# Optimization experiments

Measured on AMD Instinct MI355X. Metric: run time of the kernel, lower is better.

The kernel has to match this reference:

```python
import jax, jax.numpy as jnp
import numpy as np

TOP_K = 2

def setup_inputs() -> dict:
    key = jax.random.key(0)
    ks = jax.random.split(key, 6)
    B, S, D, F, E = 2, 2048, 1024, 4096, 8
    sd = 1.0 / np.sqrt(D)
    sf = 1.0 / np.sqrt(F)
    return {
        "x": jax.random.normal(ks[0], (B, S, D), jnp.float32),
        "gate_w": jax.random.normal(ks[1], (D, E), jnp.float32) * sd,
        "w1": jax.random.normal(ks[2], (E, D, F), jnp.float32) * sd,
        "b1": jax.random.normal(ks[3], (E, F), jnp.float32) * 0.01,
        "w2": jax.random.normal(ks[4], (E, F, D), jnp.float32) * sf,
        "b2": jax.random.normal(ks[5], (E, D), jnp.float32) * 0.01,
    }

def reference(x, gate_w, w1, b1, w2, b2):
    B, S, D = x.shape
    T = B * S
    xf = x.reshape(T, D)
    # gating: softmax over experts, top-k, renormalize
    gate_scores = jax.nn.softmax(xf @ gate_w, axis=-1)          # [T, E]
    topk_scores, topk_idx = jax.lax.top_k(gate_scores, TOP_K)    # [T, K]
    topk_scores = topk_scores / jnp.sum(topk_scores, axis=-1, keepdims=True)
    # all experts applied to all tokens (dense grouped FFN), exact erf GELU as nn.GELU
    h = jax.nn.gelu(jnp.einsum('td,edf->etf', xf, w1) + b1[:, None, :], approximate=False)  # [E,T,F]
    y = jnp.einsum('etf,efd->etd', h, w2) + b2[:, None, :]       # [E,T,D]
    # combine: gather the top-k expert outputs per token, weight and sum
    tok = jnp.arange(T)
    y_sel = y[topk_idx.T, tok[None, :]]                           # [K,T,D]
    out = jnp.einsum('kt,ktd->td', topk_scores.T, y_sel)
    return out.reshape(B, S, D)
```

## Files before the change

kernel.cpp:

```cpp
#include <hip/hip_runtime.h>
#include <hip/hip_bf16.h>
#include <stdint.h>

#define T_TOK 4096
#define D_DIM 1024
#define F_DIM 4096
#define E_NUM 8
#define NROUTED (T_TOK * 2)

typedef __attribute__((ext_vector_type(8))) __bf16 bf16x8;
typedef __attribute__((ext_vector_type(4))) float f32x4;
typedef __attribute__((ext_vector_type(8))) unsigned short u16x8;

#define WS_COUNTS 0
#define WS_CURSORS 64
#define WS_OFFSETS 128
#define WS_TOPKI 4096
#define WS_TOPKW (WS_TOPKI + NROUTED * 4)
#define WS_ROWS (WS_TOPKW + NROUTED * 4)
#define WS_DEST (WS_ROWS + NROUTED * 4)
#define WS_XB ((size_t)1 << 20)
#define WS_W1T (WS_XB + (size_t)T_TOK * D_DIM * 2)
#define WS_W2T (WS_W1T + (size_t)E_NUM * D_DIM * F_DIM * 2)
#define WS_H (WS_W2T + (size_t)E_NUM * D_DIM * F_DIM * 2)
#define WS_Y (WS_H + (size_t)NROUTED * F_DIM * 2)

__device__ __forceinline__ unsigned short f2bf(float f) {
  uint32_t u = __float_as_uint(f);
  uint32_t r = (u + 0x7FFFu + ((u >> 16) & 1u)) >> 16;
  return (unsigned short)r;
}

__device__ __forceinline__ void gll16(const void* g, void* l) {
  __builtin_amdgcn_global_load_lds(
      (__attribute__((address_space(1))) void*)(void*)(g),
      (__attribute__((address_space(3))) void*)(l), 16, 0, 0);
}

__global__ void cast_x_kernel(const float* __restrict__ x, unsigned short* __restrict__ xb) {
  int n4 = T_TOK * D_DIM / 4;
  for (int i = blockIdx.x * blockDim.x + threadIdx.x; i < n4; i += gridDim.x * blockDim.x) {
    float4 v = reinterpret_cast<const float4*>(x)[i];
    ushort4 o;
    o.x = f2bf(v.x); o.y = f2bf(v.y); o.z = f2bf(v.z); o.w = f2bf(v.w);
    reinterpret_cast<ushort4*>(xb)[i] = o;
  }
}

__global__ void transpose_cast_kernel(const float* __restrict__ src,
                                      unsigned short* __restrict__ dst, int R, int C) {
  __shared__ float tile[64][65];
  const int e = blockIdx.z;
  const int c0 = blockIdx.x * 64, r0 = blockIdx.y * 64;
  const float* s = src + (size_t)e * R * C;
  unsigned short* d = dst + (size_t)e * C * R;
  const int t = threadIdx.x;
  const int lr = t >> 4, lc = (t & 15) * 4;
#pragma unroll
  for (int rr = 0; rr < 4; rr++) {
    const int r = lr + rr * 16;
    float4 v = *reinterpret_cast<const float4*>(s + (size_t)(r0 + r) * C + c0 + lc);
    tile[r][lc + 0] = v.x; tile[r][lc + 1] = v.y;
    tile[r][lc + 2] = v.z; tile[r][lc + 3] = v.w;
  }
  __syncthreads();
  const int wc = t >> 3, wr = (t & 7) * 8;
#pragma unroll
  for (int cc = 0; cc < 2; cc++) {
    const int c = wc + cc * 32;
    u16x8 o;
#pragma unroll
    for (int k = 0; k < 8; k++) o[k] = f2bf(tile[wr + k][c]);
    *reinterpret_cast<u16x8*>(d + (size_t)(c0 + c) * R + r0 + wr) = o;
  }
}

__global__ void gate_kernel(const float* __restrict__ x, const float* __restrict__ gw,
                            int* __restrict__ topk_i, float* __restrict__ topk_w,
                            int* __restrict__ counts) {
  const int wave = threadIdx.x >> 6, lane = threadIdx.x & 63;
  const int t = blockIdx.x * 4 + wave;
  const float* xr = x + (size_t)t * D_DIM;
  double acc[E_NUM] = {0, 0, 0, 0, 0, 0, 0, 0};
  for (int d = lane; d < D_DIM; d += 64) {
    double xv = (double)xr[d];
    const float* g = gw + d * E_NUM;
#pragma unroll
    for (int e = 0; e < E_NUM; e++) acc[e] += xv * (double)g[e];
  }
#pragma unroll
  for (int off = 32; off > 0; off >>= 1) {
#pragma unroll
    for (int e = 0; e < E_NUM; e++) acc[e] += __shfl_xor(acc[e], off, 64);
  }
  if (lane == 0) {
    int i0 = 0; double b0 = acc[0];
    for (int e = 1; e < E_NUM; e++) if (acc[e] > b0) { b0 = acc[e]; i0 = e; }
    int i1 = -1; double b1v = -1e300;
    for (int e = 0; e < E_NUM; e++) if (e != i0 && acc[e] > b1v) { b1v = acc[e]; i1 = e; }
    double w0 = 1.0 / (1.0 + exp(b1v - b0));
    topk_i[t * 2] = i0; topk_i[t * 2 + 1] = i1;
    topk_w[t * 2] = (float)w0; topk_w[t * 2 + 1] = (float)(1.0 - w0);
    atomicAdd(&counts[i0], 1); atomicAdd(&counts[i1], 1);
  }
}

__global__ void scan_kernel(const int* __restrict__ counts, int* __restrict__ offsets) {
  if (threadIdx.x == 0) {
    int s = 0;
    for (int e = 0; e < E_NUM; e++) { offsets[e] = s; s += counts[e]; }
  }
}

__global__ void build_lists_kernel(const int* __restrict__ topk_i, const int* __restrict__ offsets,
                                   int* __restrict__ cursors, int* __restrict__ rows,
                                   int* __restrict__ dest) {
  int t = blockIdx.x * blockDim.x + threadIdx.x;
  if (t >= T_TOK) return;
#pragma unroll
  for (int k = 0; k < 2; k++) {
    int e = topk_i[t * 2 + k];
    int slot = atomicAdd(&cursors[e], 1);
    int r = offsets[e] + slot;
    rows[r] = t;
    dest[t * 2 + k] = r;
  }
}

__global__ __launch_bounds__(256, 3) void gemm1_kernel(
    const unsigned short* __restrict__ xb, const unsigned short* __restrict__ w1T,
    const float* __restrict__ b1, const int* __restrict__ counts,
    const int* __restrict__ offsets, const int* __restrict__ rows,
    unsigned short* __restrict__ h) {
  const int hw = blockIdx.x;
  const int lid = (hw & 7) * (8192 >> 3) + (hw >> 3);
  const int nt = lid & 31;
  const int mt = (lid >> 5) & 31;
  const int e = lid >> 10;

  const int cnt = counts[e];
  if (mt * 128 >= cnt) return;
  const int off = offsets[e];
  const int t = threadIdx.x;
  const int lane = t & 63, wave = t >> 6;
  const int wm = wave >> 1, wn = wave & 1;

  __shared__ __align__(16) unsigned short ldsA[3][4096];
  __shared__ __align__(16) unsigned short ldsB[3][4096];

  const int tr = t >> 2, tc = t & 3;
  const int a0 = mt * 128 + tr;
  const int g0 = rows[off + min(a0, cnt - 1)];
  const int g1 = rows[off + min(a0 + 64, cnt - 1)];
  const unsigned short* aptr0 = xb + (size_t)g0 * D_DIM + tc * 8;
  const unsigned short* aptr1 = xb + (size_t)g1 * D_DIM + tc * 8;
  const unsigned short* wb = w1T + (size_t)e * F_DIM * D_DIM;
  const unsigned short* bptr0 = wb + (size_t)(nt * 128 + tr) * D_DIM + tc * 8;
  const unsigned short* bptr1 = bptr0 + (size_t)64 * D_DIM;

  const int col = lane & 15;
  float bias_v[4];
#pragma unroll
  for (int nf = 0; nf < 4; nf++)
    bias_v[nf] = b1[(size_t)e * F_DIM + nt * 128 + wn * 64 + nf * 16 + col];

  f32x4 acc[4][4];
  const f32x4 z = {0.f, 0.f, 0.f, 0.f};
#pragma unroll
  for (int i = 0; i < 4; i++)
#pragma unroll
    for (int j = 0; j < 4; j++) acc[i][j] = z;

  auto stage = [&](int buf, int kt) {
    const int kb = kt * 32;
    gll16(aptr0 + kb, &ldsA[buf][wave * 512]);
    gll16(aptr1 + kb, &ldsA[buf][2048 + wave * 512]);
    gll16(bptr0 + kb, &ldsB[buf][wave * 512]);
    gll16(bptr1 + kb, &ldsB[buf][2048 + wave * 512]);
  };

  asm volatile("s_waitcnt vmcnt(0)" ::: "memory");
  stage(0, 0);
  stage(1, 1);

  const int rA = wm * 64 + (lane & 15);
  const int rB = wn * 64 + (lane & 15);
  const int ko = (lane >> 4) * 8;
  const int NK = D_DIM / 32;

  for (int kt = 0; kt < NK; ++kt) {
    const int cur = kt - (kt / 3) * 3;
    if (kt + 2 < NK) {
      stage((kt + 2) - ((kt + 2) / 3) * 3, kt + 2);
      asm volatile("s_waitcnt vmcnt(8)" ::: "memory");
    } else if (kt + 2 == NK) {
      asm volatile("s_waitcnt vmcnt(4)" ::: "memory");
    } else {
      asm volatile("s_waitcnt vmcnt(0)" ::: "memory");
    }
    __builtin_amdgcn_s_barrier();
    bf16x8 af[4], bfr[4];
#pragma unroll
    for (int mf = 0; mf < 4; mf++)
      af[mf] = *(const bf16x8*)&ldsA[cur][(rA + mf * 16) * 32 + ko];
#pragma unroll
    for (int nf = 0; nf < 4; nf++)
      bfr[nf] = *(const bf16x8*)&ldsB[cur][(rB + nf * 16) * 32 + ko];
#pragma unroll
    for (int mf = 0; mf < 4; mf++)
#pragma unroll
      for (int nf = 0; nf < 4; nf++)
        acc[mf][nf] = __builtin_amdgcn_mfma_f32_16x16x32_bf16(af[mf], bfr[nf], acc[mf][nf], 0, 0, 0);
    __builtin_amdgcn_s_barrier();
  }

  const int valid = cnt - mt * 128;
  const int rq = (lane >> 4) * 4;
#pragma unroll
  for (int nf = 0; nf < 4; nf++) {
    const int c = nt * 128 + wn * 64 + nf * 16 + col;
    const float bias = bias_v[nf];
#pragma unroll
    for (int mf = 0; mf < 4; mf++) {
#pragma unroll
      for (int r4 = 0; r4 < 4; r4++) {
        int rloc = wm * 64 + mf * 16 + rq + r4;
        if (rloc < valid) {
          float v = acc[mf][nf][r4] + bias;
          v = 0.5f * v * (1.0f + erff(v * 0.7071067811865475f));
          h[(size_t)(off + mt * 128 + rloc) * F_DIM + c] = f2bf(v);
        }
      }
    }
  }
}

__global__ __launch_bounds__(256, 3) void gemm2_kernel(
    const unsigned short* __restrict__ h, const unsigned short* __restrict__ w2T,
    const float* __restrict__ b2, const int* __restrict__ counts,
    const int* __restrict__ offsets, float* __restrict__ y) {
  const int hw = blockIdx.x;
  const int lid = (hw & 7) * (2048 >> 3) + (hw >> 3);
  const int nt = lid & 7;
  const int mt = (lid >> 3) & 31;
  const int e = lid >> 8;

  const int cnt = counts[e];
  if (mt * 128 >= cnt) return;
  const int off = offsets[e];
  const int t = threadIdx.x;
  const int lane = t & 63, wave = t >> 6;
  const int wm = wave >> 1, wn = wave & 1;

  __shared__ __align__(16) unsigned short ldsA[3][4096];
  __shared__ __align__(16) unsigned short ldsB[3][4096];

  const int tr = t >> 2, tc = t & 3;
  const int l0 = min(mt * 128 + tr, cnt - 1);
  const int l1 = min(mt * 128 + 64 + tr, cnt - 1);
  const unsigned short* aptr0 = h + (size_t)(off + l0) * F_DIM + tc * 8;
  const unsigned short* aptr1 = h + (size_t)(off + l1) * F_DIM + tc * 8;
  const unsigned short* wb = w2T + (size_t)e * D_DIM * F_DIM;
  const unsigned short* bptr0 = wb + (size_t)(nt * 128 + tr) * F_DIM + tc * 8;
  const unsigned short* bptr1 = bptr0 + (size_t)64 * F_DIM;

  const int col = lane & 15;
  float bias_v[4];
#pragma unroll
  for (int nf = 0; nf < 4; nf++)
    bias_v[nf] = b2[(size_t)e * D_DIM + nt * 128 + wn * 64 + nf * 16 + col];

  f32x4 acc[4][4];
  const f32x4 z = {0.f, 0.f, 0.f, 0.f};
#pragma unroll
  for (int i = 0; i < 4; i++)
#pragma unroll
    for (int j = 0; j < 4; j++) acc[i][j] = z;

  auto stage = [&](int buf, int kt) {
    const int kb = kt * 32;
    gll16(aptr0 + kb, &ldsA[buf][wave * 512]);
    gll16(aptr1 + kb, &ldsA[buf][2048 + wave * 512]);
    gll16(bptr0 + kb, &ldsB[buf][wave * 512]);
    gll16(bptr1 + kb, &ldsB[buf][2048 + wave * 512]);
  };

  asm volatile("s_waitcnt vmcnt(0)" ::: "memory");
  stage(0, 0);
  stage(1, 1);

  const int rA = wm * 64 + (lane & 15);
  const int rB = wn * 64 + (lane & 15);
  const int ko = (lane >> 4) * 8;
  const int NK = F_DIM / 32;

  for (int kt = 0; kt < NK; ++kt) {
    const int cur = kt - (kt / 3) * 3;
    if (kt + 2 < NK) {
      stage((kt + 2) - ((kt + 2) / 3) * 3, kt + 2);
      asm volatile("s_waitcnt vmcnt(8)" ::: "memory");
    } else if (kt + 2 == NK) {
      asm volatile("s_waitcnt vmcnt(4)" ::: "memory");
    } else {
      asm volatile("s_waitcnt vmcnt(0)" ::: "memory");
    }
    __builtin_amdgcn_s_barrier();
    bf16x8 af[4], bfr[4];
#pragma unroll
    for (int mf = 0; mf < 4; mf++)
      af[mf] = *(const bf16x8*)&ldsA[cur][(rA + mf * 16) * 32 + ko];
#pragma unroll
    for (int nf = 0; nf < 4; nf++)
      bfr[nf] = *(const bf16x8*)&ldsB[cur][(rB + nf * 16) * 32 + ko];
#pragma unroll
    for (int mf = 0; mf < 4; mf++)
#pragma unroll
      for (int nf = 0; nf < 4; nf++)
        acc[mf][nf] = __builtin_amdgcn_mfma_f32_16x16x32_bf16(af[mf], bfr[nf], acc[mf][nf], 0, 0, 0);
    __builtin_amdgcn_s_barrier();
  }

  const int valid = cnt - mt * 128;
  const int rq = (lane >> 4) * 4;
#pragma unroll
  for (int nf = 0; nf < 4; nf++) {
    const int c = nt * 128 + wn * 64 + nf * 16 + col;
    const float bias = bias_v[nf];
#pragma unroll
    for (int mf = 0; mf < 4; mf++) {
#pragma unroll
      for (int r4 = 0; r4 < 4; r4++) {
        int rloc = wm * 64 + mf * 16 + rq + r4;
        if (rloc < valid)
          y[(size_t)(off + mt * 128 + rloc) * D_DIM + c] = acc[mf][nf][r4] + bias;
      }
    }
  }
}

__global__ void combine_kernel(const float* __restrict__ y, const int* __restrict__ dest,
                               const float* __restrict__ tw, float* __restrict__ out) {
  const int n4 = T_TOK * D_DIM / 4;
  for (int i = blockIdx.x * blockDim.x + threadIdx.x; i < n4; i += gridDim.x * blockDim.x) {
    int tok = i >> 8;
    int c = i & 255;
    int r0 = dest[2 * tok], r1 = dest[2 * tok + 1];
    float w0 = tw[2 * tok], w1 = tw[2 * tok + 1];
    float4 a = reinterpret_cast<const float4*>(y + (size_t)r0 * D_DIM)[c];
    float4 b = reinterpret_cast<const float4*>(y + (size_t)r1 * D_DIM)[c];
    float4 o;
    o.x = w0 * a.x + w1 * b.x; o.y = w0 * a.y + w1 * b.y;
    o.z = w0 * a.z + w1 * b.z; o.w = w0 * a.w + w1 * b.w;
    reinterpret_cast<float4*>(out + (size_t)tok * D_DIM)[c] = o;
  }
}

extern "C" void kernel_launch(void* const* d_in, const int* in_sizes, int n_in,
                              void* d_out, int out_size, void* d_ws, size_t ws_size,
                              hipStream_t stream) {
  (void)in_sizes; (void)n_in; (void)out_size; (void)ws_size;
  const float* x = (const float*)d_in[0];
  const float* gw = (const float*)d_in[1];
  const float* w1 = (const float*)d_in[2];
  const float* b1 = (const float*)d_in[3];
  const float* w2 = (const float*)d_in[4];
  const float* b2 = (const float*)d_in[5];
  float* out = (float*)d_out;
  char* ws = (char*)d_ws;

  int* counts = (int*)(ws + WS_COUNTS);
  int* cursors = (int*)(ws + WS_CURSORS);
  int* offsets = (int*)(ws + WS_OFFSETS);
  int* topk_i = (int*)(ws + WS_TOPKI);
  float* topk_w = (float*)(ws + WS_TOPKW);
  int* rows = (int*)(ws + WS_ROWS);
  int* dest = (int*)(ws + WS_DEST);
  unsigned short* xb = (unsigned short*)(ws + WS_XB);
  unsigned short* w1T = (unsigned short*)(ws + WS_W1T);
  unsigned short* w2T = (unsigned short*)(ws + WS_W2T);
  unsigned short* hbuf = (unsigned short*)(ws + WS_H);
  float* ybuf = (float*)(ws + WS_Y);

  hipMemsetAsync(ws, 0, 4096, stream);
  cast_x_kernel<<<2048, 256, 0, stream>>>(x, xb);
  gate_kernel<<<T_TOK / 4, 256, 0, stream>>>(x, gw, topk_i, topk_w, counts);
  scan_kernel<<<1, 64, 0, stream>>>(counts, offsets);
  build_lists_kernel<<<T_TOK / 256, 256, 0, stream>>>(topk_i, offsets, cursors, rows, dest);
  transpose_cast_kernel<<<dim3(F_DIM / 64, D_DIM / 64, E_NUM), 256, 0, stream>>>(w1, w1T, D_DIM, F_DIM);
  gemm1_kernel<<<8192, 256, 0, stream>>>(xb, w1T, b1, counts, offsets, rows, hbuf);
  transpose_cast_kernel<<<dim3(D_DIM / 64, F_DIM / 64, E_NUM), 256, 0, stream>>>(w2, w2T, F_DIM, D_DIM);
  gemm2_kernel<<<2048, 256, 0, stream>>>(hbuf, w2T, b2, counts, offsets, ybuf);
  combine_kernel<<<2048, 256, 0, stream>>>(ybuf, dest, topk_w, out);
}
```

Before: 702.6 us.

## Fuse x cast into gating, deterministic compaction, swizzle LDS, stage gemm1 output via LDS

Folds the bf16 cast of x into the gate kernel and replaces the scan and atomic list build with one ballot-based compaction kernel per expert, removing two launches and an extra pass over x. Both GEMMs get an XOR swizzle on the LDS k-chunk layout to cut bank conflicts on fragment reads, and the ring-buffer index uses counters instead of modulo. The gemm1 epilogue writes GELU results into LDS and stores full 16-byte rows, which coalesces the h writes at the cost of an extra barrier. The compaction kernel walks all tokens serially per expert on one wave, which could add latency.

Result: faster. 667.4 us (-5.0%).

```diff
diff --git a/kernel.cpp b/kernel.cpp
--- a/kernel.cpp
+++ b/kernel.cpp
@@ -13,7 +13,6 @@
 typedef __attribute__((ext_vector_type(8))) unsigned short u16x8;
 
 #define WS_COUNTS 0
-#define WS_CURSORS 64
 #define WS_OFFSETS 128
 #define WS_TOPKI 4096
 #define WS_TOPKW (WS_TOPKI + NROUTED * 4)
@@ -37,16 +36,6 @@
       (__attribute__((address_space(3))) void*)(l), 16, 0, 0);
 }
 
-__global__ void cast_x_kernel(const float* __restrict__ x, unsigned short* __restrict__ xb) {
-  int n4 = T_TOK * D_DIM / 4;
-  for (int i = blockIdx.x * blockDim.x + threadIdx.x; i < n4; i += gridDim.x * blockDim.x) {
-    float4 v = reinterpret_cast<const float4*>(x)[i];
-    ushort4 o;
-    o.x = f2bf(v.x); o.y = f2bf(v.y); o.z = f2bf(v.z); o.w = f2bf(v.w);
-    reinterpret_cast<ushort4*>(xb)[i] = o;
-  }
-}
-
 __global__ void transpose_cast_kernel(const float* __restrict__ src,
                                       unsigned short* __restrict__ dst, int R, int C) {
   __shared__ float tile[64][65];
@@ -76,17 +65,27 @@
 }
 
 __global__ void gate_kernel(const float* __restrict__ x, const float* __restrict__ gw,
+                            unsigned short* __restrict__ xb,
                             int* __restrict__ topk_i, float* __restrict__ topk_w,
                             int* __restrict__ counts) {
   const int wave = threadIdx.x >> 6, lane = threadIdx.x & 63;
   const int t = blockIdx.x * 4 + wave;
   const float* xr = x + (size_t)t * D_DIM;
+  unsigned short* xo = xb + (size_t)t * D_DIM;
   double acc[E_NUM] = {0, 0, 0, 0, 0, 0, 0, 0};
-  for (int d = lane; d < D_DIM; d += 64) {
-    double xv = (double)xr[d];
-    const float* g = gw + d * E_NUM;
-#pragma unroll
-    for (int e = 0; e < E_NUM; e++) acc[e] += xv * (double)g[e];
+#pragma unroll
+  for (int it = 0; it < D_DIM / 256; it++) {
+    const int d0 = it * 256 + lane * 4;
+    float4 v = *reinterpret_cast<const float4*>(xr + d0);
+    ushort4 o;
+    o.x = f2bf(v.x); o.y = f2bf(v.y); o.z = f2bf(v.z); o.w = f2bf(v.w);
+    *reinterpret_cast<ushort4*>(xo + d0) = o;
+    const float* g = gw + (size_t)d0 * E_NUM;
+    float xv[4] = {v.x, v.y, v.z, v.w};
+#pragma unroll
+    for (int j = 0; j < 4; j++)
+#pragma unroll
+      for (int e = 0; e < E_NUM; e++) acc[e] += (double)xv[j] * (double)g[j * E_NUM + e];
   }
 #pragma unroll
   for (int off = 32; off > 0; off >>= 1) {
@@ -105,27 +104,30 @@
   }
 }
 
-__global__ void scan_kernel(const int* __restrict__ counts, int* __restrict__ offsets) {
-  if (threadIdx.x == 0) {
-    int s = 0;
-    for (int e = 0; e < E_NUM; e++) { offsets[e] = s; s += counts[e]; }
-  }
-}
-
-__global__ void build_lists_kernel(const int* __restrict__ topk_i, const int* __restrict__ offsets,
-                                   int* __restrict__ cursors, int* __restrict__ rows,
-                                   int* __restrict__ dest) {
-  int t = blockIdx.x * blockDim.x + threadIdx.x;
-  if (t >= T_TOK) return;
-#pragma unroll
-  for (int k = 0; k < 2; k++) {
-    int e = topk_i[t * 2 + k];
-    int slot = atomicAdd(&cursors[e], 1);
-    int r = offsets[e] + slot;
-    rows[r] = t;
-    dest[t * 2 + k] = r;
-  }
-}
+__global__ void compact_kernel(const int* __restrict__ topk_i, const int* __restrict__ counts,
+                               int* __restrict__ offsets, int* __restrict__ rows,
+                               int* __restrict__ dest) {
+  const int e = blockIdx.x;
+  const int lane = threadIdx.x;
+  int offv = 0;
+  for (int i = 0; i < e; i++) offv += counts[i];
+  if (lane == 0) offsets[e] = offv;
+  int run = 0;
+  for (int c = 0; c < T_TOK; c += 64) {
+    const int t = c + lane;
+    const int i0 = topk_i[2 * t], i1 = topk_i[2 * t + 1];
+    const bool hit = (i0 == e) || (i1 == e);
+    unsigned long long m = __ballot(hit);
+    int pre = __popcll(m & ((1ull << lane) - 1ull));
+    if (hit) {
+      int r = offv + run + pre;
+      rows[r] = t;
+      dest[2 * t + (i0 == e ? 0 : 1)] = r;
+    }
+    run += __popcll(m);
+  }
+}
+
 
 __global__ __launch_bounds__(256, 3) void gemm1_kernel(
     const unsigned short* __restrict__ xb, const unsigned short* __restrict__ w1T,
@@ -145,17 +147,19 @@
   const int lane = t & 63, wave = t >> 6;
   const int wm = wave >> 1, wn = wave & 1;
 
-  __shared__ __align__(16) unsigned short ldsA[3][4096];
-  __shared__ __align__(16) unsigned short ldsB[3][4096];
-
-  const int tr = t >> 2, tc = t & 3;
+  __shared__ __align__(16) unsigned short lds[24576];
+  unsigned short* ldsA = lds;
+  unsigned short* ldsB = lds + 12288;
+
+  const int tr = t >> 2;
+  const int tcs = (t & 3) ^ ((t >> 3) & 3);
   const int a0 = mt * 128 + tr;
   const int g0 = rows[off + min(a0, cnt - 1)];
   const int g1 = rows[off + min(a0 + 64, cnt - 1)];
-  const unsigned short* aptr0 = xb + (size_t)g0 * D_DIM + tc * 8;
-  const unsigned short* aptr1 = xb + (size_t)g1 * D_DIM + tc * 8;
+  const unsigned short* aptr0 = xb + (size_t)g0 * D_DIM + tcs * 8;
+  const unsigned short* aptr1 = xb + (size_t)g1 * D_DIM + tcs * 8;
   const unsigned short* wb = w1T + (size_t)e * F_DIM * D_DIM;
-  const unsigned short* bptr0 = wb + (size_t)(nt * 128 + tr) * D_DIM + tc * 8;
+  const unsigned short* bptr0 = wb + (size_t)(nt * 128 + tr) * D_DIM + tcs * 8;
   const unsigned short* bptr1 = bptr0 + (size_t)64 * D_DIM;
 
   const int col = lane & 15;
@@ -173,10 +177,10 @@
 
   auto stage = [&](int buf, int kt) {
     const int kb = kt * 32;
-    gll16(aptr0 + kb, &ldsA[buf][wave * 512]);
-    gll16(aptr1 + kb, &ldsA[buf][2048 + wave * 512]);
-    gll16(bptr0 + kb, &ldsB[buf][wave * 512]);
-    gll16(bptr1 + kb, &ldsB[buf][2048 + wave * 512]);
+    gll16(aptr0 + kb, ldsA + buf * 4096 + wave * 512);
+    gll16(aptr1 + kb, ldsA + buf * 4096 + 2048 + wave * 512);
+    gll16(bptr0 + kb, ldsB + buf * 4096 + wave * 512);
+    gll16(bptr1 + kb, ldsB + buf * 4096 + 2048 + wave * 512);
   };
 
   asm volatile("s_waitcnt vmcnt(0)" ::: "memory");
@@ -185,13 +189,13 @@
 
   const int rA = wm * 64 + (lane & 15);
   const int rB = wn * 64 + (lane & 15);
-  const int ko = (lane >> 4) * 8;
+  const int ko = (((lane >> 4) ^ ((lane >> 1) & 3)) * 8);
   const int NK = D_DIM / 32;
 
+  int cur = 0, nxt = 2;
   for (int kt = 0; kt < NK; ++kt) {
-    const int cur = kt - (kt / 3) * 3;
     if (kt + 2 < NK) {
-      stage((kt + 2) - ((kt + 2) / 3) * 3, kt + 2);
+      stage(nxt, kt + 2);
       asm volatile("s_waitcnt vmcnt(8)" ::: "memory");
     } else if (kt + 2 == NK) {
       asm volatile("s_waitcnt vmcnt(4)" ::: "memory");
@@ -202,35 +206,48 @@
     bf16x8 af[4], bfr[4];
 #pragma unroll
     for (int mf = 0; mf < 4; mf++)
-      af[mf] = *(const bf16x8*)&ldsA[cur][(rA + mf * 16) * 32 + ko];
+      af[mf] = *(const bf16x8*)&ldsA[cur * 4096 + (rA + mf * 16) * 32 + ko];
 #pragma unroll
     for (int nf = 0; nf < 4; nf++)
-      bfr[nf] = *(const bf16x8*)&ldsB[cur][(rB + nf * 16) * 32 + ko];
+      bfr[nf] = *(const bf16x8*)&ldsB[cur * 4096 + (rB + nf * 16) * 32 + ko];
 #pragma unroll
     for (int mf = 0; mf < 4; mf++)
 #pragma unroll
       for (int nf = 0; nf < 4; nf++)
         acc[mf][nf] = __builtin_amdgcn_mfma_f32_16x16x32_bf16(af[mf], bfr[nf], acc[mf][nf], 0, 0, 0);
     __builtin_amdgcn_s_barrier();
-  }
+    cur = (cur == 2) ? 0 : cur + 1;
+    nxt = (nxt == 2) ? 0 : nxt + 1;
+  }
+
+  __syncthreads();
 
   const int valid = cnt - mt * 128;
   const int rq = (lane >> 4) * 4;
 #pragma unroll
   for (int nf = 0; nf < 4; nf++) {
-    const int c = nt * 128 + wn * 64 + nf * 16 + col;
     const float bias = bias_v[nf];
 #pragma unroll
     for (int mf = 0; mf < 4; mf++) {
 #pragma unroll
       for (int r4 = 0; r4 < 4; r4++) {
-        int rloc = wm * 64 + mf * 16 + rq + r4;
-        if (rloc < valid) {
-          float v = acc[mf][nf][r4] + bias;
-          v = 0.5f * v * (1.0f + erff(v * 0.7071067811865475f));
-          h[(size_t)(off + mt * 128 + rloc) * F_DIM + c] = f2bf(v);
-        }
+        int r = wm * 64 + mf * 16 + rq + r4;
+        int c = wn * 64 + nf * 16 + col;
+        float v = acc[mf][nf][r4] + bias;
+        v = 0.5f * v * (1.0f + erff(v * 0.7071067811865475f));
+        lds[r * 136 + c] = f2bf(v);
       }
+    }
+  }
+  __syncthreads();
+  const int srow = t >> 4;
+  const int scol = (t & 15) * 8;
+#pragma unroll
+  for (int i = 0; i < 8; i++) {
+    int r = srow + i * 16;
+    if (r < valid) {
+      u16x8 v = *(const u16x8*)&lds[r * 136 + scol];
+      *(u16x8*)&h[(size_t)(off + mt * 128 + r) * F_DIM + nt * 128 + scol] = v;
     }
   }
 }
@@ -255,13 +272,14 @@
   __shared__ __align__(16) unsigned short ldsA[3][4096];
   __shared__ __align__(16) unsigned short ldsB[3][4096];
 
-  const int tr = t >> 2, tc = t & 3;
+  const int tr = t >> 2;
+  const int tcs = (t & 3) ^ ((t >> 3) & 3);
   const int l0 = min(mt * 128 + tr, cnt - 1);
   const int l1 = min(mt * 128 + 64 + tr, cnt - 1);
-  const unsigned short* aptr0 = h + (size_t)(off + l0) * F_DIM + tc * 8;
-  const unsigned short* aptr1 = h + (size_t)(off + l1) * F_DIM + tc * 8;
+  const unsigned short* aptr0 = h + (size_t)(off + l0) * F_DIM + tcs * 8;
+  const unsigned short* aptr1 = h + (size_t)(off + l1) * F_DIM + tcs * 8;
   const unsigned short* wb = w2T + (size_t)e * D_DIM * F_DIM;
-  const unsigned short* bptr0 = wb + (size_t)(nt * 128 + tr) * F_DIM + tc * 8;
+  const unsigned short* bptr0 = wb + (size_t)(nt * 128 + tr) * F_DIM + tcs * 8;
   const unsigned short* bptr1 = bptr0 + (size_t)64 * F_DIM;
 
   const int col = lane & 15;
@@ -291,13 +309,13 @@
 
   const int rA = wm * 64 + (lane & 15);
   const int rB = wn * 64 + (lane & 15);
-  const int ko = (lane >> 4) * 8;
+  const int ko = (((lane >> 4) ^ ((lane >> 1) & 3)) * 8);
   const int NK = F_DIM / 32;
 
+  int cur = 0, nxt = 2;
   for (int kt = 0; kt < NK; ++kt) {
-    const int cur = kt - (kt / 3) * 3;
     if (kt + 2 < NK) {
-      stage((kt + 2) - ((kt + 2) / 3) * 3, kt + 2);
+      stage(nxt, kt + 2);
       asm volatile("s_waitcnt vmcnt(8)" ::: "memory");
     } else if (kt + 2 == NK) {
       asm volatile("s_waitcnt vmcnt(4)" ::: "memory");
@@ -318,6 +336,8 @@
       for (int nf = 0; nf < 4; nf++)
         acc[mf][nf] = __builtin_amdgcn_mfma_f32_16x16x32_bf16(af[mf], bfr[nf], acc[mf][nf], 0, 0, 0);
     __builtin_amdgcn_s_barrier();
+    cur = (cur == 2) ? 0 : cur + 1;
+    nxt = (nxt == 2) ? 0 : nxt + 1;
   }
 
   const int valid = cnt - mt * 128;
@@ -369,7 +389,6 @@
   char* ws = (char*)d_ws;
 
   int* counts = (int*)(ws + WS_COUNTS);
-  int* cursors = (int*)(ws + WS_CURSORS);
   int* offsets = (int*)(ws + WS_OFFSETS);
   int* topk_i = (int*)(ws + WS_TOPKI);
   float* topk_w = (float*)(ws + WS_TOPKW);
@@ -382,10 +401,8 @@
   float* ybuf = (float*)(ws + WS_Y);
 
   hipMemsetAsync(ws, 0, 4096, stream);
-  cast_x_kernel<<<2048, 256, 0, stream>>>(x, xb);
-  gate_kernel<<<T_TOK / 4, 256, 0, stream>>>(x, gw, topk_i, topk_w, counts);
-  scan_kernel<<<1, 64, 0, stream>>>(counts, offsets);
-  build_lists_kernel<<<T_TOK / 256, 256, 0, stream>>>(topk_i, offsets, cursors, rows, dest);
+  gate_kernel<<<T_TOK / 4, 256, 0, stream>>>(x, gw, xb, topk_i, topk_w, counts);
+  compact_kernel<<<E_NUM, 64, 0, stream>>>(topk_i, counts, offsets, rows, dest);
   transpose_cast_kernel<<<dim3(F_DIM / 64, D_DIM / 64, E_NUM), 256, 0, stream>>>(w1, w1T, D_DIM, F_DIM);
   gemm1_kernel<<<8192, 256, 0, stream>>>(xb, w1T, b1, counts, offsets, rows, hbuf);
   transpose_cast_kernel<<<dim3(D_DIM / 64, F_DIM / 64, E_NUM), 256, 0, stream>>>(w2, w2T, F_DIM, D_DIM);
```
